# Kernel optimization log

Hardware: AMD Instinct MI355X
Metric: run time of the kernel (lower is better)

## Reference

```python
import jax, jax.numpy as jnp
import numpy as np

EPS = 1e-5

def layer_norm(x, gamma, beta):
    mu = jnp.mean(x, axis=-1, keepdims=True)
    var = jnp.var(x, axis=-1, keepdims=True)
    return (x - mu) * jax.lax.rsqrt(var + EPS) * gamma + beta

def setup_inputs() -> dict:
    key = jax.random.key(0)
    ks = jax.random.split(key, 5)
    B, C, H, W = 4, 256, 64, 64
    x = jax.random.normal(ks[0], (B, C, H, W), dtype=jnp.float32)
    gamma = jnp.ones((C,), dtype=jnp.float32)
    beta = jnp.zeros((C,), dtype=jnp.float32)
    s = 1.0 / np.sqrt(C)
    Wq = jax.random.normal(ks[1], (C, C), dtype=jnp.float32) * s
    Wk = jax.random.normal(ks[2], (C, C), dtype=jnp.float32) * s
    Wv = jax.random.normal(ks[3], (C, C), dtype=jnp.float32) * s
    w1 = jnp.ones((1,), dtype=jnp.float32)
    w2 = jnp.ones((1,), dtype=jnp.float32)
    return {"x": x, "gamma": gamma, "beta": beta, "Wq": Wq, "Wk": Wk, "Wv": Wv, "w1": w1, "w2": w2}

def reference(x, gamma, beta, Wq, Wk, Wv, w1, w2):
    B, C, H, W = x.shape
    # [B,C,H,W] -> tokens [B,N,C]
    xn = layer_norm(x.reshape(B, C, H * W).transpose(0, 2, 1), gamma, beta)
    Q = xn @ Wq  # [B,N,C]
    K = xn @ Wk
    V = xn @ Wv
    S = jnp.einsum('bnc,bmc->bnm', Q, K)  # [B,N,N]
    attn1 = jax.nn.softmax(S, axis=-1)
    attn2 = jnp.square(jax.nn.relu(S))
    e1 = jnp.exp(w1)
    e2 = jnp.exp(w2)
    a1 = e1 / (e1 + e2)
    a2 = e2 / (e1 + e2)
    attn = a1 * attn1 + a2 * attn2
    out = jnp.einsum('bnm,bmc->bnc', attn, V)  # [B,N,C]
    out = out.transpose(0, 2, 1).reshape(B, C, H, W)
    res = xn.transpose(0, 2, 1).reshape(B, C, H, W)
    return out + res
```

## Files before the change

kernel.cpp:

```cpp
#include <hip/hip_runtime.h>
#include <hip/hip_bf16.h>
#include <cstdint>

typedef unsigned short u16;
typedef __attribute__((ext_vector_type(8))) short bf16x8;
typedef __attribute__((ext_vector_type(4))) float f32x4;

#define BATCH 4
#define CDIM 256
#define NTOK 4096

__device__ inline float fexp2(float x) { return __builtin_amdgcn_exp2f(x); }

__device__ inline u16 f2bf(float f) {
  union { float f; uint32_t u; } un; un.f = f;
  uint32_t u = un.u;
  u += 0x7fffu + ((u >> 16) & 1u);
  return (u16)(u >> 16);
}
__device__ inline float bf2f(u16 h) {
  union { uint32_t u; float f; } un; un.u = ((uint32_t)h) << 16; return un.f;
}

__device__ inline void gload_lds16(const u16* g, u16* l) {
  __builtin_amdgcn_global_load_lds((const __attribute__((address_space(1))) void*)g,
                                   (__attribute__((address_space(3))) void*)l, 16, 0, 0);
}

__global__ __launch_bounds__(256) void ln_kernel(const float* __restrict__ x,
                                                 const float* __restrict__ gamma,
                                                 const float* __restrict__ beta,
                                                 u16* __restrict__ xn) {
  __shared__ float tile[CDIM][33];
  __shared__ float reds[8][32];
  __shared__ float reds2[8][32];
  __shared__ float mu_s[32], rs_s[32];

  int b  = blockIdx.x >> 7;
  int n0 = (blockIdx.x & 127) * 32;
  const float* xb = x + (size_t)b * CDIM * NTOK;

  int t = threadIdx.x & 31;
  int g = threadIdx.x >> 5;

  for (int c = g; c < CDIM; c += 8)
    tile[c][t] = xb[(size_t)c * NTOK + n0 + t];
  __syncthreads();

  float s = 0.f, s2 = 0.f;
  for (int c = g * 32; c < g * 32 + 32; ++c) {
    float v = tile[c][t];
    s += v; s2 += v * v;
  }
  reds[g][t] = s; reds2[g][t] = s2;
  __syncthreads();
  if (threadIdx.x < 32) {
    float ts = 0.f, ts2 = 0.f;
    for (int gg = 0; gg < 8; ++gg) { ts += reds[gg][threadIdx.x]; ts2 += reds2[gg][threadIdx.x]; }
    float mu = ts / CDIM;
    float var = ts2 / CDIM - mu * mu;
    mu_s[threadIdx.x] = mu;
    rs_s[threadIdx.x] = rsqrtf(var + 1e-5f);
  }
  __syncthreads();

  int c = threadIdx.x;
  float gam = gamma[c], bet = beta[c];
  u16* out = xn + ((size_t)b * NTOK + n0) * CDIM;
  for (int tt = 0; tt < 32; ++tt) {
    float v = tile[c][tt];
    float y = (v - mu_s[tt]) * rs_s[tt] * gam + bet;
    out[(size_t)tt * CDIM + c] = f2bf(y);
  }
}

__global__ __launch_bounds__(256) void wt_kernel(const float* __restrict__ W,
                                                 u16* __restrict__ WT,
                                                 float scale) {
  __shared__ float tile[32][33];
  int i0 = blockIdx.y * 32;
  int j0 = blockIdx.x * 32;
  int tx = threadIdx.x, ty = threadIdx.y;
  for (int r = ty; r < 32; r += 8)
    tile[r][tx] = W[(size_t)(i0 + r) * CDIM + j0 + tx];
  __syncthreads();
  for (int r = ty; r < 32; r += 8)
    WT[(size_t)(j0 + r) * CDIM + i0 + tx] = f2bf(tile[tx][r] * scale);
}

__global__ __launch_bounds__(256) void qkv_kernel(const u16* __restrict__ A,
                                                  const u16* __restrict__ B3,
                                                  u16* __restrict__ Qb,
                                                  u16* __restrict__ Kb,
                                                  u16* __restrict__ VT) {
  constexpr int BM = 128, BN = 64, BK = 32;
  __shared__ u16 shA[BM][BK + 8];
  __shared__ u16 shB[BN][BK + 8];

  int m0 = blockIdx.y * BM;
  int n0 = blockIdx.x * BN;

  int tid  = threadIdx.x;
  int lane = tid & 63;
  int wave = tid >> 6;
  int wm = wave >> 1, wn = wave & 1;
  int col  = lane & 15;
  int quad = lane >> 4;

  f32x4 acc[4][2];
#pragma unroll
  for (int i = 0; i < 4; ++i)
#pragma unroll
    for (int j = 0; j < 2; ++j) acc[i][j] = (f32x4){0.f, 0.f, 0.f, 0.f};

  for (int kb = 0; kb < CDIM; kb += BK) {
    __syncthreads();
#pragma unroll
    for (int c = tid; c < BM * BK / 8; c += 256) {
      int row = c >> 2, kc = c & 3;
      *(uint4*)&shA[row][kc * 8] = *(const uint4*)&A[(size_t)(m0 + row) * CDIM + kb + kc * 8];
    }
#pragma unroll
    for (int c = tid; c < BN * BK / 8; c += 256) {
      int row = c >> 2, kc = c & 3;
      *(uint4*)&shB[row][kc * 8] = *(const uint4*)&B3[(size_t)(n0 + row) * CDIM + kb + kc * 8];
    }
    __syncthreads();

    bf16x8 af[4], bfv[2];
#pragma unroll
    for (int i = 0; i < 4; ++i)
      af[i] = *(const bf16x8*)&shA[wm * 64 + i * 16 + col][quad * 8];
#pragma unroll
    for (int j = 0; j < 2; ++j)
      bfv[j] = *(const bf16x8*)&shB[wn * 32 + j * 16 + col][quad * 8];
#pragma unroll
    for (int i = 0; i < 4; ++i)
#pragma unroll
      for (int j = 0; j < 2; ++j)
        acc[i][j] = __builtin_amdgcn_mfma_f32_16x16x32_bf16(af[i], bfv[j], acc[i][j], 0, 0, 0);
  }

  int mode = n0 >> 8;
  int r0 = quad * 4;
#pragma unroll
  for (int i = 0; i < 4; ++i) {
    int mbase = m0 + wm * 64 + i * 16 + r0;
#pragma unroll
    for (int j = 0; j < 2; ++j) {
      int n = n0 + wn * 32 + j * 16 + col;
#pragma unroll
      for (int r = 0; r < 4; ++r) {
        int m = mbase + r;
        float v = acc[i][j][r];
        if (mode == 0) {
          Qb[(size_t)m * CDIM + n] = f2bf(v);
        } else if (mode == 1) {
          Kb[(size_t)m * CDIM + (n - 256)] = f2bf(v);
        } else {
          int cv = n - 512, bb = m >> 12, nt = m & 4095;
          VT[((size_t)bb * CDIM + cv) * NTOK + nt] = f2bf(v);
        }
      }
    }
  }
}


#define P1_STEP(KF)                                                            \
  {                                                                            \
    f32x4 s0 = (f32x4){0.f, 0.f, 0.f, 0.f};                                    \
    f32x4 s1 = (f32x4){0.f, 0.f, 0.f, 0.f};                                    \
    _Pragma("unroll")                                                          \
    for (int kk = 0; kk < 8; ++kk) {                                           \
      s0 = __builtin_amdgcn_mfma_f32_16x16x32_bf16(aq[0][kk], KF[kk], s0, 0, 0, 0); \
      s1 = __builtin_amdgcn_mfma_f32_16x16x32_bf16(aq[1][kk], KF[kk], s1, 0, 0, 0); \
    }                                                                          \
    float mn0[4], mn1[4];                                                      \
    bool chg = false;                                                          \
    _Pragma("unroll")                                                          \
    for (int r = 0; r < 4; ++r) {                                              \
      mn0[r] = fmaxf(ml[0][r], s0[r]);                                         \
      mn1[r] = fmaxf(ml[1][r], s1[r]);                                         \
      chg = chg || (mn0[r] > ml[0][r]) || (mn1[r] > ml[1][r]);                 \
    }                                                                          \
    if (__any(chg)) {                                                          \
      _Pragma("unroll")                                                        \
      for (int r = 0; r < 4; ++r) {                                            \
        ll[0][r] = ll[0][r] * fexp2(ml[0][r] - mn0[r]) + fexp2(s0[r] - mn0[r]);\
        ml[0][r] = mn0[r];                                                     \
        ll[1][r] = ll[1][r] * fexp2(ml[1][r] - mn1[r]) + fexp2(s1[r] - mn1[r]);\
        ml[1][r] = mn1[r];                                                     \
      }                                                                        \
    } else {                                                                   \
      _Pragma("unroll")                                                        \
      for (int r = 0; r < 4; ++r) {                                            \
        ll[0][r] += fexp2(s0[r] - ml[0][r]);                                   \
        ll[1][r] += fexp2(s1[r] - ml[1][r]);                                   \
      }                                                                        \
    }                                                                          \
  }

#define S_COMPUTE(BK_)                                                         \
  {                                                                            \
    s0 = (f32x4){0.f, 0.f, 0.f, 0.f};                                          \
    s1 = (f32x4){0.f, 0.f, 0.f, 0.f};                                          \
    _Pragma("unroll")                                                          \
    for (int kk = 0; kk < 8; ++kk) {                                           \
      s0 = __builtin_amdgcn_mfma_f32_16x16x32_bf16(aq[0][kk], BK_[kk], s0, 0, 0, 0); \
      s1 = __builtin_amdgcn_mfma_f32_16x16x32_bf16(aq[1][kk], BK_[kk], s1, 0, 0, 0); \
    }                                                                          \
  }

#define P2_WRITE(PN)                                                           \
  {                                                                            \
    _Pragma("unroll")                                                          \
    for (int r = 0; r < 4; ++r) {                                              \
      float sv0 = s0[r];                                                       \
      float rl0 = sv0 > 0.f ? sv0 * sv0 : 0.f;                                 \
      float p0v = c1[0][r] * fexp2(sv0 - mf[0][r]) + a2p * rl0;                \
      (PN)[(quad * 4 + r) * 40 + w * 16 + col] = f2bf(p0v);                    \
      float sv1 = s1[r];                                                       \
      float rl1 = sv1 > 0.f ? sv1 * sv1 : 0.f;                                 \
      float p1v = c1[1][r] * fexp2(sv1 - mf[1][r]) + a2p * rl1;                \
      (PN)[(16 + quad * 4 + r) * 40 + w * 16 + col] = f2bf(p1v);               \
    }                                                                          \
  }

__global__ __launch_bounds__(256, 2) void fa_kernel(const u16* __restrict__ Qg,
                                                    const u16* __restrict__ Kg,
                                                    const u16* __restrict__ Vtg,
                                                    const u16* __restrict__ xng,
                                                    const float* __restrict__ w1p,
                                                    const float* __restrict__ w2p,
                                                    float* __restrict__ outg) {
  __shared__ __align__(16) char smem[71680];
  float* otile = (float*)smem;
  u16* pb0 = (u16*)(smem + 65536);
  u16* pb1 = (u16*)(smem + 68096);
  float* mbuf = (float*)(smem + 70656);
  float* lbuf = (float*)(smem + 71168);

  int b  = blockIdx.x & 3;
  int q0 = (blockIdx.x >> 2) * 32;

  const u16* Q  = Qg  + (size_t)b * NTOK * CDIM;
  const u16* K  = Kg  + (size_t)b * NTOK * CDIM;
  const u16* Vt = Vtg + (size_t)b * NTOK * CDIM;

  int tid  = threadIdx.x;
  int lane = tid & 63;
  int w    = tid >> 6;
  int col = lane & 15, quad = lane >> 4;

  float e1 = __expf(w1p[0]), e2 = __expf(w2p[0]);
  float a1 = e1 / (e1 + e2), a2 = e2 / (e1 + e2);
  float a2p = a2 * 0.4804530139182014f;

  bf16x8 aq[2][8];
#pragma unroll
  for (int g = 0; g < 2; ++g)
#pragma unroll
    for (int kk = 0; kk < 8; ++kk)
      aq[g][kk] = *(const bf16x8*)&Q[(size_t)(q0 + g * 16 + col) * CDIM + kk * 32 + quad * 8];

  int koff1[8];
#pragma unroll
  for (int it = 0; it < 8; ++it) {
    int row = it * 8 + (tid >> 5);
    int ch  = (tid & 31) ^ (row & 31);
    koff1[it] = row * CDIM + ch * 8;
  }
  int koff2[4], voff2[4];
#pragma unroll
  for (int it = 0; it < 4; ++it) {
    int row = it * 8 + (tid >> 5);
    int ch  = (tid & 31) ^ row;
    koff2[it] = row * CDIM + ch * 8;
    int vr  = it * 64 + (tid >> 2);
    int vch = (tid & 3) ^ ((vr >> 1) & 3);
    voff2[it] = vr * NTOK + vch * 8;
  }

  u16* ka = (u16*)smem;
  u16* kb = ka + 16384;

  auto stage1 = [&](int n1, u16* Kdst) {
    const u16* kgb = K + (size_t)n1 * CDIM;
#pragma unroll
    for (int it = 0; it < 8; ++it)
      gload_lds16(kgb + koff1[it], Kdst + (size_t)(it * 256 + w * 64) * 8);
  };

  stage1(0, ka);

  float ml[2][4], ll[2][4];
#pragma unroll
  for (int g = 0; g < 2; ++g)
#pragma unroll
    for (int r = 0; r < 4; ++r) { ml[g][r] = -3e38f; ll[g][r] = 0.f; }

  __syncthreads();

  int kr1 = w * 16 + col;
  for (int t = 0; t < 64; ++t) {
    if (t < 63) stage1((t + 1) * 64, kb);

    bf16x8 bkf[8];
#pragma unroll
    for (int kk = 0; kk < 8; ++kk)
      bkf[kk] = *(const bf16x8*)&ka[(size_t)kr1 * 256 + (((kk * 4 + quad) ^ kr1) & 31) * 8];
    P1_STEP(bkf)

    __syncthreads();
    u16* tk = ka; ka = kb; kb = tk;
  }

#pragma unroll
  for (int off = 1; off < 16; off <<= 1)
#pragma unroll
    for (int g = 0; g < 2; ++g)
#pragma unroll
      for (int r = 0; r < 4; ++r) {
        float mo = __shfl_xor(ml[g][r], off);
        float lo = __shfl_xor(ll[g][r], off);
        float mn = fmaxf(ml[g][r], mo);
        ll[g][r] = ll[g][r] * fexp2(ml[g][r] - mn) + lo * fexp2(mo - mn);
        ml[g][r] = mn;
      }
  if (col == 0) {
#pragma unroll
    for (int g = 0; g < 2; ++g)
#pragma unroll
      for (int r = 0; r < 4; ++r) {
        int qr = g * 16 + quad * 4 + r;
        mbuf[w * 32 + qr] = ml[g][r];
        lbuf[w * 32 + qr] = ll[g][r];
      }
  }
  __syncthreads();
  float mf[2][4], c1[2][4];
#pragma unroll
  for (int g = 0; g < 2; ++g)
#pragma unroll
    for (int r = 0; r < 4; ++r) {
      int qr = g * 16 + quad * 4 + r;
      float M = -3e38f, L = 0.f;
#pragma unroll
      for (int ww = 0; ww < 4; ++ww) {
        float mo = mbuf[ww * 32 + qr];
        float lo = lbuf[ww * 32 + qr];
        float mn = fmaxf(M, mo);
        L = L * fexp2(M - mn) + lo * fexp2(mo - mn);
        M = mn;
      }
      mf[g][r] = M;
      c1[g][r] = a1 / L;
    }

  u16* k2a = (u16*)smem;
  u16* k2b = k2a + 8192;
  u16* v2a = (u16*)(smem + 32768);
  u16* v2b = v2a + 8192;

  auto stageK2 = [&](int n1, u16* Kdst) {
    const u16* kgb = K + (size_t)n1 * CDIM;
#pragma unroll
    for (int it = 0; it < 4; ++it)
      gload_lds16(kgb + koff2[it], Kdst + (size_t)(it * 256 + w * 64) * 8);
  };
  auto stageV2 = [&](int n1, u16* Vdst) {
    const u16* vgb = Vt + n1;
#pragma unroll
    for (int it = 0; it < 4; ++it)
      gload_lds16(vgb + voff2[it], Vdst + (size_t)(it * 256 + w * 64) * 8);
  };

  f32x4 o[2][8];
#pragma unroll
  for (int g = 0; g < 2; ++g)
#pragma unroll
    for (int j = 0; j < 8; ++j) o[g][j] = (f32x4){0.f, 0.f, 0.f, 0.f};

  int kr2 = w * 16 + col;
  int c2  = w - 2;

  stageK2(0, k2a);
  __syncthreads();
  if (w < 2) {
    bf16x8 bk[8];
#pragma unroll
    for (int kk = 0; kk < 8; ++kk)
      bk[kk] = *(const bf16x8*)&k2a[(size_t)kr2 * 256 + (((kk * 4 + quad) ^ kr2) & 31) * 8];
    f32x4 s0, s1;
    S_COMPUTE(bk)
    P2_WRITE(pb0)
  }
  stageK2(32, k2b);
  stageV2(0, v2a);
  __syncthreads();

  for (int t = 0; t < 128; ++t) {
    if (t < 126) stageK2((t + 2) * 32, (t & 1) ? k2b : k2a);
    if (t < 127) stageV2((t + 1) * 32, ((t + 1) & 1) ? v2b : v2a);

    if (w < 2) {
      if (t < 127) {
        const u16* ksrc = ((t + 1) & 1) ? k2b : k2a;
        bf16x8 bk[8];
#pragma unroll
        for (int kk = 0; kk < 8; ++kk)
          bk[kk] = *(const bf16x8*)&ksrc[(size_t)kr2 * 256 + (((kk * 4 + quad) ^ kr2) & 31) * 8];
        f32x4 s0, s1;
        S_COMPUTE(bk)
        u16* pdst = ((t + 1) & 1) ? pb1 : pb0;
        P2_WRITE(pdst)
      }
    } else {
      const u16* psrc = (t & 1) ? pb1 : pb0;
      const u16* vsrc = (t & 1) ? v2b : v2a;
      bf16x8 pa0 = *(const bf16x8*)&psrc[(size_t)(col) * 40 + quad * 8];
      bf16x8 pa1 = *(const bf16x8*)&psrc[(size_t)(16 + col) * 40 + quad * 8];
#pragma unroll
      for (int j = 0; j < 8; ++j) {
        int vr = c2 * 128 + j * 16 + col;
        bf16x8 bv = *(const bf16x8*)&vsrc[(size_t)vr * 32 + (quad ^ ((vr >> 1) & 3)) * 8];
        o[0][j] = __builtin_amdgcn_mfma_f32_16x16x32_bf16(pa0, bv, o[0][j], 0, 0, 0);
        o[1][j] = __builtin_amdgcn_mfma_f32_16x16x32_bf16(pa1, bv, o[1][j], 0, 0, 0);
      }
    }
    __syncthreads();
  }

  if (w >= 2) {
#pragma unroll
    for (int g = 0; g < 2; ++g)
#pragma unroll
      for (int j = 0; j < 8; ++j) {
        int c = c2 * 128 + j * 16 + col;
        float4 v4;
        float* vv = (float*)&v4;
#pragma unroll
        for (int r = 0; r < 4; ++r) {
          int row = g * 16 + quad * 4 + r;
          vv[r] = o[g][j][r] + bf2f(xng[((size_t)b * NTOK + q0 + row) * CDIM + c]);
        }
        *(float4*)&otile[(size_t)c * 36 + g * 16 + quad * 4] = v4;
      }
  }
  __syncthreads();

#pragma unroll
  for (int it = 0; it < 8; ++it) {
    int c  = it * 32 + (tid >> 3);
    int ch = tid & 7;
    *(float4*)&outg[((size_t)b * CDIM + c) * NTOK + q0 + ch * 4] =
        *(const float4*)&otile[(size_t)c * 36 + ch * 4];
  }
}

extern "C" void kernel_launch(void* const* d_in, const int* in_sizes, int n_in,
                              void* d_out, int out_size, void* d_ws, size_t ws_size,
                              hipStream_t stream) {
  const float* x     = (const float*)d_in[0];
  const float* gamma = (const float*)d_in[1];
  const float* beta  = (const float*)d_in[2];
  const float* Wq    = (const float*)d_in[3];
  const float* Wk    = (const float*)d_in[4];
  const float* Wv    = (const float*)d_in[5];
  const float* w1    = (const float*)d_in[6];
  const float* w2    = (const float*)d_in[7];
  float* out = (float*)d_out;

  char* ws = (char*)d_ws;
  size_t off = 0;
  u16* xn  = (u16*)(ws + off); off += (size_t)BATCH * NTOK * CDIM * 2;
  u16* WT3 = (u16*)(ws + off); off += (size_t)3 * CDIM * CDIM * 2;
  u16* Qb  = (u16*)(ws + off); off += (size_t)BATCH * NTOK * CDIM * 2;
  u16* Kb  = (u16*)(ws + off); off += (size_t)BATCH * NTOK * CDIM * 2;
  u16* VT  = (u16*)(ws + off); off += (size_t)BATCH * NTOK * CDIM * 2;

  const float LOG2E = 1.4426950408889634f;

  ln_kernel<<<dim3(BATCH * (NTOK / 32)), 256, 0, stream>>>(x, gamma, beta, xn);

  wt_kernel<<<dim3(8, 8), dim3(32, 8), 0, stream>>>(Wq, WT3, LOG2E);
  wt_kernel<<<dim3(8, 8), dim3(32, 8), 0, stream>>>(Wk, WT3 + 256 * 256, 1.0f);
  wt_kernel<<<dim3(8, 8), dim3(32, 8), 0, stream>>>(Wv, WT3 + 512 * 256, 1.0f);

  qkv_kernel<<<dim3(12, 128), 256, 0, stream>>>(xn, WT3, Qb, Kb, VT);

  fa_kernel<<<dim3(512), 256, 0, stream>>>(Qb, Kb, VT, xn, w1, w2, out);
}
```

Baseline: 299.2 us.

## Give each wave private LDS buffers and replace block barriers with vmcnt waits

Each wave now stages only the K rows (or V columns) it consumes into its own private double-buffered LDS region, prefetching two tiles ahead. In the first pass this removes the per-iteration __syncthreads, relying instead on s_waitcnt vmcnt/lgkmcnt to know when its own loads have landed. The second pass keeps one barrier per step only for the P-tile handoff between the producer and consumer waves. It also hoists all V fragment reads ahead of the MFMAs and raises wave priority around the MFMA blocks. The risk is ordering bugs from the hand-placed waitcnts, plus more VGPRs held for prefetched fragments.

New measurement: 298.5 us. Within noise of the previous version (-0.2%).

```diff
diff --git a/kernel.cpp b/kernel.cpp
--- a/kernel.cpp
+++ b/kernel.cpp
@@ -25,6 +25,14 @@
 __device__ inline void gload_lds16(const u16* g, u16* l) {
   __builtin_amdgcn_global_load_lds((const __attribute__((address_space(1))) void*)g,
                                    (__attribute__((address_space(3))) void*)l, 16, 0, 0);
+}
+
+__device__ inline void wait_vm8()   { asm volatile("s_waitcnt vmcnt(8)" ::: "memory"); }
+__device__ inline void wait_vm0()   { asm volatile("s_waitcnt vmcnt(0)" ::: "memory"); }
+__device__ inline void wait_lgkm0() { asm volatile("s_waitcnt lgkmcnt(0)" ::: "memory"); }
+__device__ inline void barrier_lgkm() {
+  asm volatile("s_waitcnt lgkmcnt(0)\n\ts_barrier" ::: "memory");
+  __builtin_amdgcn_sched_barrier(0);
 }
 
 __global__ __launch_bounds__(256) void ln_kernel(const float* __restrict__ x,
@@ -227,6 +235,11 @@
     }                                                                          \
   }
 
+#define RD_KFRAG(FR, BUFP)                                                     \
+  _Pragma("unroll")                                                            \
+  for (int kk = 0; kk < 8; ++kk)                                               \
+    FR[kk] = *(const bf16x8*)((BUFP) + col * 256 + (((kk * 4 + quad) ^ col) & 31) * 8);
+
 __global__ __launch_bounds__(256, 2) void fa_kernel(const u16* __restrict__ Qg,
                                                     const u16* __restrict__ Kg,
                                                     const u16* __restrict__ Vtg,
@@ -253,6 +266,8 @@
   int w    = tid >> 6;
   int col = lane & 15, quad = lane >> 4;
 
+  u16* myreg = (u16*)(smem + w * 16384);
+
   float e1 = __expf(w1p[0]), e2 = __expf(w2p[0]);
   float a1 = e1 / (e1 + e2), a2 = e2 / (e1 + e2);
   float a2p = a2 * 0.4804530139182014f;
@@ -264,35 +279,35 @@
     for (int kk = 0; kk < 8; ++kk)
       aq[g][kk] = *(const bf16x8*)&Q[(size_t)(q0 + g * 16 + col) * CDIM + kk * 32 + quad * 8];
 
-  int koff1[8];
+  int koffK[8];
 #pragma unroll
   for (int it = 0; it < 8; ++it) {
-    int row = it * 8 + (tid >> 5);
-    int ch  = (tid & 31) ^ (row & 31);
-    koff1[it] = row * CDIM + ch * 8;
-  }
-  int koff2[4], voff2[4];
-#pragma unroll
-  for (int it = 0; it < 4; ++it) {
-    int row = it * 8 + (tid >> 5);
-    int ch  = (tid & 31) ^ row;
-    koff2[it] = row * CDIM + ch * 8;
-    int vr  = it * 64 + (tid >> 2);
-    int vch = (tid & 3) ^ ((vr >> 1) & 3);
-    voff2[it] = vr * NTOK + vch * 8;
-  }
-
-  u16* ka = (u16*)smem;
-  u16* kb = ka + 16384;
-
-  auto stage1 = [&](int n1, u16* Kdst) {
+    int rl = it * 2 + (lane >> 5);
+    int g8 = (lane & 31) ^ rl;
+    koffK[it] = (w * 16 + rl) * CDIM + g8 * 8;
+  }
+  int voffV[8];
+#pragma unroll
+  for (int it = 0; it < 8; ++it) {
+    int vrl = it * 16 + (lane >> 2);
+    int g3 = (lane & 3) ^ ((vrl >> 1) & 3);
+    voffV[it] = ((w - 2) * 128 + vrl) * NTOK + g3 * 8;
+  }
+
+  auto stK = [&](int n1, int bufsel) {
     const u16* kgb = K + (size_t)n1 * CDIM;
+    u16* dst = myreg + bufsel * 4096;
 #pragma unroll
     for (int it = 0; it < 8; ++it)
-      gload_lds16(kgb + koff1[it], Kdst + (size_t)(it * 256 + w * 64) * 8);
+      gload_lds16(kgb + koffK[it], dst + it * 512);
   };
-
-  stage1(0, ka);
+  auto stV = [&](int n1, int bufsel) {
+    const u16* vgb = Vt + n1;
+    u16* dst = myreg + bufsel * 4096;
+#pragma unroll
+    for (int it = 0; it < 8; ++it)
+      gload_lds16(vgb + voffV[it], dst + it * 512);
+  };
 
   float ml[2][4], ll[2][4];
 #pragma unroll
@@ -300,21 +315,20 @@
 #pragma unroll
     for (int r = 0; r < 4; ++r) { ml[g][r] = -3e38f; ll[g][r] = 0.f; }
 
-  __syncthreads();
-
-  int kr1 = w * 16 + col;
+  stK(0, 0);
+  stK(64, 1);
+
   for (int t = 0; t < 64; ++t) {
-    if (t < 63) stage1((t + 1) * 64, kb);
-
-    bf16x8 bkf[8];
-#pragma unroll
-    for (int kk = 0; kk < 8; ++kk)
-      bkf[kk] = *(const bf16x8*)&ka[(size_t)kr1 * 256 + (((kk * 4 + quad) ^ kr1) & 31) * 8];
-    P1_STEP(bkf)
-
-    __syncthreads();
-    u16* tk = ka; ka = kb; kb = tk;
-  }
+    if (t < 63) wait_vm8(); else wait_vm0();
+    bf16x8 fr[8];
+    RD_KFRAG(fr, myreg + (t & 1) * 4096)
+    wait_lgkm0();
+    if (t < 62) stK((t + 2) * 64, t & 1);
+    P1_STEP(fr)
+  }
+
+  if (w < 2) { stK(0, 0); stK(32, 1); }
+  else       { stV(0, 0); stV(32, 1); }
 
 #pragma unroll
   for (int off = 1; off < 16; off <<= 1)
@@ -358,81 +372,66 @@
       c1[g][r] = a1 / L;
     }
 
-  u16* k2a = (u16*)smem;
-  u16* k2b = k2a + 8192;
-  u16* v2a = (u16*)(smem + 32768);
-  u16* v2b = v2a + 8192;
-
-  auto stageK2 = [&](int n1, u16* Kdst) {
-    const u16* kgb = K + (size_t)n1 * CDIM;
-#pragma unroll
-    for (int it = 0; it < 4; ++it)
-      gload_lds16(kgb + koff2[it], Kdst + (size_t)(it * 256 + w * 64) * 8);
-  };
-  auto stageV2 = [&](int n1, u16* Vdst) {
-    const u16* vgb = Vt + n1;
-#pragma unroll
-    for (int it = 0; it < 4; ++it)
-      gload_lds16(vgb + voff2[it], Vdst + (size_t)(it * 256 + w * 64) * 8);
-  };
-
   f32x4 o[2][8];
 #pragma unroll
   for (int g = 0; g < 2; ++g)
 #pragma unroll
     for (int j = 0; j < 8; ++j) o[g][j] = (f32x4){0.f, 0.f, 0.f, 0.f};
 
-  int kr2 = w * 16 + col;
-  int c2  = w - 2;
-
-  stageK2(0, k2a);
-  __syncthreads();
   if (w < 2) {
-    bf16x8 bk[8];
-#pragma unroll
-    for (int kk = 0; kk < 8; ++kk)
-      bk[kk] = *(const bf16x8*)&k2a[(size_t)kr2 * 256 + (((kk * 4 + quad) ^ kr2) & 31) * 8];
+    wait_vm0();
+    bf16x8 fr[8];
+    RD_KFRAG(fr, myreg)
+    wait_lgkm0();
+    stK(2 * 32, 0);
     f32x4 s0, s1;
-    S_COMPUTE(bk)
+    S_COMPUTE(fr)
     P2_WRITE(pb0)
   }
-  stageK2(32, k2b);
-  stageV2(0, v2a);
-  __syncthreads();
+  barrier_lgkm();
 
   for (int t = 0; t < 128; ++t) {
-    if (t < 126) stageK2((t + 2) * 32, (t & 1) ? k2b : k2a);
-    if (t < 127) stageV2((t + 1) * 32, ((t + 1) & 1) ? v2b : v2a);
-
     if (w < 2) {
       if (t < 127) {
-        const u16* ksrc = ((t + 1) & 1) ? k2b : k2a;
-        bf16x8 bk[8];
-#pragma unroll
-        for (int kk = 0; kk < 8; ++kk)
-          bk[kk] = *(const bf16x8*)&ksrc[(size_t)kr2 * 256 + (((kk * 4 + quad) ^ kr2) & 31) * 8];
+        if (t < 126) wait_vm8(); else wait_vm0();
+        bf16x8 fr[8];
+        RD_KFRAG(fr, myreg + ((t + 1) & 1) * 4096)
+        wait_lgkm0();
+        if (t < 125) stK((t + 3) * 32, (t + 1) & 1);
         f32x4 s0, s1;
-        S_COMPUTE(bk)
-        u16* pdst = ((t + 1) & 1) ? pb1 : pb0;
-        P2_WRITE(pdst)
+        __builtin_amdgcn_s_setprio(1);
+        S_COMPUTE(fr)
+        __builtin_amdgcn_s_setprio(0);
+        P2_WRITE(((t + 1) & 1) ? pb1 : pb0)
       }
     } else {
+      if (t < 127) wait_vm8(); else wait_vm0();
       const u16* psrc = (t & 1) ? pb1 : pb0;
-      const u16* vsrc = (t & 1) ? v2b : v2a;
-      bf16x8 pa0 = *(const bf16x8*)&psrc[(size_t)(col) * 40 + quad * 8];
-      bf16x8 pa1 = *(const bf16x8*)&psrc[(size_t)(16 + col) * 40 + quad * 8];
+      const u16* vsrc = myreg + (t & 1) * 4096;
+      bf16x8 pa0 = *(const bf16x8*)&psrc[col * 40 + quad * 8];
+      bf16x8 pa1 = *(const bf16x8*)&psrc[(16 + col) * 40 + quad * 8];
+      bf16x8 bvf[8];
 #pragma unroll
       for (int j = 0; j < 8; ++j) {
-        int vr = c2 * 128 + j * 16 + col;
-        bf16x8 bv = *(const bf16x8*)&vsrc[(size_t)vr * 32 + (quad ^ ((vr >> 1) & 3)) * 8];
-        o[0][j] = __builtin_amdgcn_mfma_f32_16x16x32_bf16(pa0, bv, o[0][j], 0, 0, 0);
-        o[1][j] = __builtin_amdgcn_mfma_f32_16x16x32_bf16(pa1, bv, o[1][j], 0, 0, 0);
-      }
+        int vrl = j * 16 + col;
+        bvf[j] = *(const bf16x8*)&vsrc[vrl * 32 + ((quad ^ ((vrl >> 1) & 3)) & 3) * 8];
+      }
+      wait_lgkm0();
+      if (t < 126) stV((t + 2) * 32, t & 1);
+      __builtin_amdgcn_s_setprio(1);
+#pragma unroll
+      for (int j = 0; j < 8; ++j) {
+        o[0][j] = __builtin_amdgcn_mfma_f32_16x16x32_bf16(pa0, bvf[j], o[0][j], 0, 0, 0);
+        o[1][j] = __builtin_amdgcn_mfma_f32_16x16x32_bf16(pa1, bvf[j], o[1][j], 0, 0, 0);
+      }
+      __builtin_amdgcn_s_setprio(0);
     }
-    __syncthreads();
-  }
-
+    barrier_lgkm();
+  }
+
+  __syncthreads();
   if (w >= 2) {
+    int c2 = w - 2;
 #pragma unroll
     for (int g = 0; g < 2; ++g)
 #pragma unroll
```

## Double query tile to 64 rows with 512-thread blocks sharing K/V loads

Applied to the files above, without the earlier changes.

The attention kernel now processes 64 query rows per block using 8 waves instead of 32 rows with 4 waves. Staged K and V tiles are shared across twice as many queries, which halves global K/V traffic per query. The consumer waves compute 4x4 MFMA tiles, giving more reuse per operand load. s_setprio hints are also added around the MFMA sections. The cost is more LDS per block, an extra barrier, fewer blocks in the grid, and possible occupancy or register pressure at 512 threads.

Measured after the change: 284.0 us. 5.1% less time.

```diff
diff --git a/kernel.cpp b/kernel.cpp
--- a/kernel.cpp
+++ b/kernel.cpp
@@ -219,30 +219,30 @@
       float sv0 = s0[r];                                                       \
       float rl0 = sv0 > 0.f ? sv0 * sv0 : 0.f;                                 \
       float p0v = c1[0][r] * fexp2(sv0 - mf[0][r]) + a2p * rl0;                \
-      (PN)[(quad * 4 + r) * 40 + w * 16 + col] = f2bf(p0v);                    \
+      (PN)[(qh * 32 + quad * 4 + r) * 40 + kh * 16 + col] = f2bf(p0v);         \
       float sv1 = s1[r];                                                       \
       float rl1 = sv1 > 0.f ? sv1 * sv1 : 0.f;                                 \
       float p1v = c1[1][r] * fexp2(sv1 - mf[1][r]) + a2p * rl1;                \
-      (PN)[(16 + quad * 4 + r) * 40 + w * 16 + col] = f2bf(p1v);               \
+      (PN)[(qh * 32 + 16 + quad * 4 + r) * 40 + kh * 16 + col] = f2bf(p1v);    \
     }                                                                          \
   }
 
-__global__ __launch_bounds__(256, 2) void fa_kernel(const u16* __restrict__ Qg,
+__global__ __launch_bounds__(512, 2) void fa_kernel(const u16* __restrict__ Qg,
                                                     const u16* __restrict__ Kg,
                                                     const u16* __restrict__ Vtg,
                                                     const u16* __restrict__ xng,
                                                     const float* __restrict__ w1p,
                                                     const float* __restrict__ w2p,
                                                     float* __restrict__ outg) {
-  __shared__ __align__(16) char smem[71680];
+  __shared__ __align__(16) char smem[77824];
   float* otile = (float*)smem;
   u16* pb0 = (u16*)(smem + 65536);
-  u16* pb1 = (u16*)(smem + 68096);
-  float* mbuf = (float*)(smem + 70656);
-  float* lbuf = (float*)(smem + 71168);
+  u16* pb1 = (u16*)(smem + 70656);
+  float* mbuf = (float*)(smem + 75776);
+  float* lbuf = (float*)(smem + 76800);
 
   int b  = blockIdx.x & 3;
-  int q0 = (blockIdx.x >> 2) * 32;
+  int q0 = (blockIdx.x >> 2) * 64;
 
   const u16* Q  = Qg  + (size_t)b * NTOK * CDIM;
   const u16* K  = Kg  + (size_t)b * NTOK * CDIM;
@@ -253,6 +253,12 @@
   int w    = tid >> 6;
   int col = lane & 15, quad = lane >> 4;
 
+  int qh = w >> 2;
+  int kq = w & 3;
+  bool isProd = (w & 2) == 0;
+  int kh = w & 1;
+  int c4 = (w & 1) + 2 * (w >> 2);
+
   float e1 = __expf(w1p[0]), e2 = __expf(w2p[0]);
   float a1 = e1 / (e1 + e2), a2 = e2 / (e1 + e2);
   float a2p = a2 * 0.4804530139182014f;
@@ -262,36 +268,53 @@
   for (int g = 0; g < 2; ++g)
 #pragma unroll
     for (int kk = 0; kk < 8; ++kk)
-      aq[g][kk] = *(const bf16x8*)&Q[(size_t)(q0 + g * 16 + col) * CDIM + kk * 32 + quad * 8];
-
-  int koff1[8];
-#pragma unroll
-  for (int it = 0; it < 8; ++it) {
-    int row = it * 8 + (tid >> 5);
+      aq[g][kk] = *(const bf16x8*)&Q[(size_t)(q0 + qh * 32 + g * 16 + col) * CDIM +
+                                     kk * 32 + quad * 8];
+
+  int koff1[4];
+#pragma unroll
+  for (int it = 0; it < 4; ++it) {
+    int row = it * 16 + (tid >> 5);
     int ch  = (tid & 31) ^ (row & 31);
     koff1[it] = row * CDIM + ch * 8;
   }
-  int koff2[4], voff2[4];
-#pragma unroll
-  for (int it = 0; it < 4; ++it) {
-    int row = it * 8 + (tid >> 5);
+  int koff2[2];
+#pragma unroll
+  for (int it = 0; it < 2; ++it) {
+    int row = it * 16 + (tid >> 5);
     int ch  = (tid & 31) ^ row;
     koff2[it] = row * CDIM + ch * 8;
-    int vr  = it * 64 + (tid >> 2);
-    int vch = (tid & 3) ^ ((vr >> 1) & 3);
-    voff2[it] = vr * NTOK + vch * 8;
-  }
+  }
+  int voff2[2];
+#pragma unroll
+  for (int it = 0; it < 2; ++it) {
+    int vr = it * 128 + (tid >> 2);
+    int g3 = (tid & 3) ^ ((vr >> 1) & 3);
+    voff2[it] = vr * NTOK + g3 * 8;
+  }
+
+  auto stage1 = [&](int n1, u16* dst) {
+    const u16* kgb = K + (size_t)n1 * CDIM;
+#pragma unroll
+    for (int it = 0; it < 4; ++it)
+      gload_lds16(kgb + koff1[it], dst + it * 4096 + (tid >> 6) * 512 + lane * 8);
+  };
+  auto stageK2 = [&](int n1, u16* dst) {
+    const u16* kgb = K + (size_t)n1 * CDIM;
+#pragma unroll
+    for (int it = 0; it < 2; ++it)
+      gload_lds16(kgb + koff2[it], dst + it * 4096 + (tid >> 6) * 512 + lane * 8);
+  };
+  auto stageV2 = [&](int n1, u16* dst) {
+    const u16* vgb = Vt + n1;
+#pragma unroll
+    for (int it = 0; it < 2; ++it)
+      gload_lds16(vgb + voff2[it], dst + it * 4096 + (tid >> 6) * 512 + lane * 8);
+  };
 
   u16* ka = (u16*)smem;
   u16* kb = ka + 16384;
 
-  auto stage1 = [&](int n1, u16* Kdst) {
-    const u16* kgb = K + (size_t)n1 * CDIM;
-#pragma unroll
-    for (int it = 0; it < 8; ++it)
-      gload_lds16(kgb + koff1[it], Kdst + (size_t)(it * 256 + w * 64) * 8);
-  };
-
   stage1(0, ka);
 
   float ml[2][4], ll[2][4];
@@ -302,7 +325,7 @@
 
   __syncthreads();
 
-  int kr1 = w * 16 + col;
+  int kr1 = kq * 16 + col;
   for (int t = 0; t < 64; ++t) {
     if (t < 63) stage1((t + 1) * 64, kb);
 
@@ -334,8 +357,8 @@
 #pragma unroll
       for (int r = 0; r < 4; ++r) {
         int qr = g * 16 + quad * 4 + r;
-        mbuf[w * 32 + qr] = ml[g][r];
-        lbuf[w * 32 + qr] = ll[g][r];
+        mbuf[qh * 128 + kq * 32 + qr] = ml[g][r];
+        lbuf[qh * 128 + kq * 32 + qr] = ll[g][r];
       }
   }
   __syncthreads();
@@ -347,9 +370,9 @@
       int qr = g * 16 + quad * 4 + r;
       float M = -3e38f, L = 0.f;
 #pragma unroll
-      for (int ww = 0; ww < 4; ++ww) {
-        float mo = mbuf[ww * 32 + qr];
-        float lo = lbuf[ww * 32 + qr];
+      for (int k2 = 0; k2 < 4; ++k2) {
+        float mo = mbuf[qh * 128 + k2 * 32 + qr];
+        float lo = lbuf[qh * 128 + k2 * 32 + qr];
         float mn = fmaxf(M, mo);
         L = L * fexp2(M - mn) + lo * fexp2(mo - mn);
         M = mn;
@@ -357,37 +380,24 @@
       mf[g][r] = M;
       c1[g][r] = a1 / L;
     }
+  __syncthreads();
 
   u16* k2a = (u16*)smem;
   u16* k2b = k2a + 8192;
   u16* v2a = (u16*)(smem + 32768);
   u16* v2b = v2a + 8192;
 
-  auto stageK2 = [&](int n1, u16* Kdst) {
-    const u16* kgb = K + (size_t)n1 * CDIM;
-#pragma unroll
-    for (int it = 0; it < 4; ++it)
-      gload_lds16(kgb + koff2[it], Kdst + (size_t)(it * 256 + w * 64) * 8);
-  };
-  auto stageV2 = [&](int n1, u16* Vdst) {
-    const u16* vgb = Vt + n1;
-#pragma unroll
-    for (int it = 0; it < 4; ++it)
-      gload_lds16(vgb + voff2[it], Vdst + (size_t)(it * 256 + w * 64) * 8);
-  };
-
-  f32x4 o[2][8];
-#pragma unroll
-  for (int g = 0; g < 2; ++g)
-#pragma unroll
-    for (int j = 0; j < 8; ++j) o[g][j] = (f32x4){0.f, 0.f, 0.f, 0.f};
-
-  int kr2 = w * 16 + col;
-  int c2  = w - 2;
+  f32x4 o[4][4];
+#pragma unroll
+  for (int i = 0; i < 4; ++i)
+#pragma unroll
+    for (int j = 0; j < 4; ++j) o[i][j] = (f32x4){0.f, 0.f, 0.f, 0.f};
+
+  int kr2 = kh * 16 + col;
 
   stageK2(0, k2a);
   __syncthreads();
-  if (w < 2) {
+  if (isProd) {
     bf16x8 bk[8];
 #pragma unroll
     for (int kk = 0; kk < 8; ++kk)
@@ -404,7 +414,7 @@
     if (t < 126) stageK2((t + 2) * 32, (t & 1) ? k2b : k2a);
     if (t < 127) stageV2((t + 1) * 32, ((t + 1) & 1) ? v2b : v2a);
 
-    if (w < 2) {
+    if (isProd) {
       if (t < 127) {
         const u16* ksrc = ((t + 1) & 1) ? k2b : k2a;
         bf16x8 bk[8];
@@ -412,50 +422,59 @@
         for (int kk = 0; kk < 8; ++kk)
           bk[kk] = *(const bf16x8*)&ksrc[(size_t)kr2 * 256 + (((kk * 4 + quad) ^ kr2) & 31) * 8];
         f32x4 s0, s1;
+        __builtin_amdgcn_s_setprio(1);
         S_COMPUTE(bk)
-        u16* pdst = ((t + 1) & 1) ? pb1 : pb0;
-        P2_WRITE(pdst)
+        __builtin_amdgcn_s_setprio(0);
+        P2_WRITE(((t + 1) & 1) ? pb1 : pb0)
       }
     } else {
       const u16* psrc = (t & 1) ? pb1 : pb0;
       const u16* vsrc = (t & 1) ? v2b : v2a;
-      bf16x8 pa0 = *(const bf16x8*)&psrc[(size_t)(col) * 40 + quad * 8];
-      bf16x8 pa1 = *(const bf16x8*)&psrc[(size_t)(16 + col) * 40 + quad * 8];
-#pragma unroll
-      for (int j = 0; j < 8; ++j) {
-        int vr = c2 * 128 + j * 16 + col;
-        bf16x8 bv = *(const bf16x8*)&vsrc[(size_t)vr * 32 + (quad ^ ((vr >> 1) & 3)) * 8];
-        o[0][j] = __builtin_amdgcn_mfma_f32_16x16x32_bf16(pa0, bv, o[0][j], 0, 0, 0);
-        o[1][j] = __builtin_amdgcn_mfma_f32_16x16x32_bf16(pa1, bv, o[1][j], 0, 0, 0);
-      }
+      bf16x8 pa[4];
+#pragma unroll
+      for (int i = 0; i < 4; ++i)
+        pa[i] = *(const bf16x8*)&psrc[(size_t)(i * 16 + col) * 40 + quad * 8];
+      bf16x8 bv[4];
+#pragma unroll
+      for (int j = 0; j < 4; ++j) {
+        int vr = c4 * 64 + j * 16 + col;
+        bv[j] = *(const bf16x8*)&vsrc[(size_t)vr * 32 + ((quad ^ ((vr >> 1) & 3)) & 3) * 8];
+      }
+      __builtin_amdgcn_s_setprio(1);
+#pragma unroll
+      for (int i = 0; i < 4; ++i)
+#pragma unroll
+        for (int j = 0; j < 4; ++j)
+          o[i][j] = __builtin_amdgcn_mfma_f32_16x16x32_bf16(pa[i], bv[j], o[i][j], 0, 0, 0);
+      __builtin_amdgcn_s_setprio(0);
     }
     __syncthreads();
   }
 
-  if (w >= 2) {
-#pragma unroll
-    for (int g = 0; g < 2; ++g)
-#pragma unroll
-      for (int j = 0; j < 8; ++j) {
-        int c = c2 * 128 + j * 16 + col;
+  if (!isProd) {
+#pragma unroll
+    for (int i = 0; i < 4; ++i)
+#pragma unroll
+      for (int j = 0; j < 4; ++j) {
+        int c = c4 * 64 + j * 16 + col;
         float4 v4;
         float* vv = (float*)&v4;
 #pragma unroll
         for (int r = 0; r < 4; ++r) {
-          int row = g * 16 + quad * 4 + r;
-          vv[r] = o[g][j][r] + bf2f(xng[((size_t)b * NTOK + q0 + row) * CDIM + c]);
+          int row = i * 16 + quad * 4 + r;
+          vv[r] = o[i][j][r] + bf2f(xng[((size_t)b * NTOK + q0 + row) * CDIM + c]);
         }
-        *(float4*)&otile[(size_t)c * 36 + g * 16 + quad * 4] = v4;
+        *(float4*)&otile[(size_t)c * 68 + i * 16 + quad * 4] = v4;
       }
   }
   __syncthreads();
 
 #pragma unroll
   for (int it = 0; it < 8; ++it) {
-    int c  = it * 32 + (tid >> 3);
-    int ch = tid & 7;
-    *(float4*)&outg[((size_t)b * CDIM + c) * NTOK + q0 + ch * 4] =
-        *(const float4*)&otile[(size_t)c * 36 + ch * 4];
+    int c  = it * 32 + (tid >> 4);
+    int n4 = tid & 15;
+    *(float4*)&outg[((size_t)b * CDIM + c) * NTOK + q0 + n4 * 4] =
+        *(const float4*)&otile[(size_t)c * 68 + n4 * 4];
   }
 }
 
@@ -490,5 +509,5 @@
 
   qkv_kernel<<<dim3(12, 128), 256, 0, stream>>>(xn, WT3, Qb, Kb, VT);
 
-  fa_kernel<<<dim3(512), 256, 0, stream>>>(Qb, Kb, VT, xn, w1, w2, out);
-}
+  fa_kernel<<<dim3(256), 512, 0, stream>>>(Qb, Kb, VT, xn, w1, w2, out);
+}
```
